# Optimization experiments

Hardware: AMD Instinct MI355X
Metric: run time of the kernel (lower is better)

## Reference

```python
import jax, jax.numpy as jnp
import numpy as np

WIDTH = 1024
NUM_BLOCKS = 16
BLOCK_W = WIDTH // NUM_BLOCKS
C_VALUE = 8.0
D_VALUE = 1.0
LN_EPS = 1e-6  # flax nn.LayerNorm default


def setup_inputs() -> dict:
    key = jax.random.key(0)
    kx, kw, ka = jax.random.split(key, 3)
    x = jax.random.normal(kx, (4, 8192, WIDTH), dtype=jnp.float32)
    # BlockDiagonalLinear params (variance_scaling fan_in normal ~ std=1/sqrt(block_w))
    w = jax.random.normal(kw, (NUM_BLOCKS, BLOCK_W, BLOCK_W), dtype=jnp.float32) / np.sqrt(BLOCK_W)
    b = jnp.zeros((NUM_BLOCKS, BLOCK_W), dtype=jnp.float32)
    # LayerNorm params
    ln_scale = jnp.ones((WIDTH,), dtype=jnp.float32)
    ln_bias = jnp.zeros((WIDTH,), dtype=jnp.float32)
    # a_param: rnn_param_init on ring [0.9, 0.999] with softplus transform
    unif = jax.random.uniform(ka, (WIDTH,))
    a_real = 0.5 * jnp.log(unif * (0.999 ** 2 - 0.9 ** 2) + 0.9 ** 2 + 1e-8)
    a_param = jnp.log(jnp.exp(-a_real) - 1.0).astype(jnp.float32)
    return {"x": x, "ln_scale": ln_scale, "ln_bias": ln_bias, "w": w, "b": b, "a_param": a_param}


def reference(x, ln_scale, ln_bias, w, b, a_param):
    # LayerNorm over last axis
    mean = jnp.mean(x, axis=-1, keepdims=True)
    var = jnp.mean(jnp.square(x - mean), axis=-1, keepdims=True)
    xn = (x - mean) * jax.lax.rsqrt(var + LN_EPS) * ln_scale + ln_bias
    # Block-diagonal linear: [..., (h i)] -> [..., h, i] @ [h, i, j] -> [..., (h j)]
    xb = xn.reshape(*xn.shape[:-1], NUM_BLOCKS, BLOCK_W)
    yb = jnp.einsum('bshi,hij->bshj', xb, w) + b
    gate_input = yb.reshape(*x.shape[:-1], WIDTH)
    # gate chain
    log_a = -C_VALUE * jax.nn.sigmoid(D_VALUE * gate_input) * jax.nn.softplus(a_param)
    alpha = jnp.exp(log_a)
    alpha = jnp.clip(alpha, 0.05, 0.95)  # gate_type == 'gru'
    beta = 1.0 - alpha
    return (alpha, beta)
```

## Files before the change

### kernel.cpp

```cpp
#include <hip/hip_runtime.h>

#define WIDTH 1024
#define BW 64
#define NB 16
#define ROWS 8
#define HPAD 68
#define ROWSTRIDE (NB * HPAD)

__global__ __launch_bounds__(512, 6)
void griffin_gate_kernel(const float* __restrict__ x,
                         const float* __restrict__ ln_scale,
                         const float* __restrict__ ln_bias,
                         const float* __restrict__ w,
                         const float* __restrict__ b,
                         const float* __restrict__ a_param,
                         float* __restrict__ alpha_out,
                         float* __restrict__ beta_out)
{
    __shared__ float xn_s[ROWS * ROWSTRIDE];

    const int t    = threadIdx.x;
    const int wave = t >> 6;
    const int lane = t & 63;
    const long long row_base = (long long)blockIdx.x * ROWS;

    const int h   = t >> 5;
    const int jl  = (t & 31) * 2;
    const int col = h * BW + jl;
    const float2 bias2 = *(const float2*)(b + col);
    const float2 ap    = *(const float2*)(a_param + col);
    float2 sp;
    sp.x = log1pf(__expf(ap.x));
    sp.y = log1pf(__expf(ap.y));

    {
        const float* xrow = x + (row_base + wave) * WIDTH;
        float4 v[4];
        float s = 0.f, s2 = 0.f;
#pragma unroll
        for (int k = 0; k < 4; ++k) {
            v[k] = *(const float4*)(xrow + 256 * k + 4 * lane);
            s += v[k].x + v[k].y + v[k].z + v[k].w;
            s2 = fmaf(v[k].x, v[k].x, s2);
            s2 = fmaf(v[k].y, v[k].y, s2);
            s2 = fmaf(v[k].z, v[k].z, s2);
            s2 = fmaf(v[k].w, v[k].w, s2);
        }
#pragma unroll
        for (int off = 32; off >= 1; off >>= 1) {
            s  += __shfl_xor(s,  off, 64);
            s2 += __shfl_xor(s2, off, 64);
        }
        const float mean = s * (1.0f / WIDTH);
        const float var  = fmaxf(s2 * (1.0f / WIDTH) - mean * mean, 0.0f);
        const float rstd = rsqrtf(var + 1e-6f);
#pragma unroll
        for (int k = 0; k < 4; ++k) {
            const float4 sc = *(const float4*)(ln_scale + 256 * k + 4 * lane);
            const float4 bi = *(const float4*)(ln_bias  + 256 * k + 4 * lane);
            float4 xn;
            xn.x = fmaf((v[k].x - mean) * rstd, sc.x, bi.x);
            xn.y = fmaf((v[k].y - mean) * rstd, sc.y, bi.y);
            xn.z = fmaf((v[k].z - mean) * rstd, sc.z, bi.z);
            xn.w = fmaf((v[k].w - mean) * rstd, sc.w, bi.w);
            const int hh    = 4 * k + (lane >> 4);
            const int inner = 4 * (lane & 15);
            *(float4*)(&xn_s[wave * ROWSTRIDE + hh * HPAD + inner]) = xn;
        }
    }
    __syncthreads();

    float2 acc[ROWS];
#pragma unroll
    for (int r = 0; r < ROWS; ++r) acc[r] = bias2;

    const float* wh = w + h * (BW * BW) + jl;
    const float* xs = xn_s + h * HPAD;
#pragma unroll 4
    for (int i4 = 0; i4 < 16; ++i4) {
        const float* wp = wh + i4 * 4 * BW;
        const float2 w0 = *(const float2*)(wp);
        const float2 w1 = *(const float2*)(wp + BW);
        const float2 w2 = *(const float2*)(wp + 2 * BW);
        const float2 w3 = *(const float2*)(wp + 3 * BW);
#pragma unroll
        for (int r = 0; r < ROWS; ++r) {
            const float4 xq = *(const float4*)(xs + r * ROWSTRIDE + i4 * 4);
            acc[r].x = fmaf(xq.x, w0.x, acc[r].x);
            acc[r].y = fmaf(xq.x, w0.y, acc[r].y);
            acc[r].x = fmaf(xq.y, w1.x, acc[r].x);
            acc[r].y = fmaf(xq.y, w1.y, acc[r].y);
            acc[r].x = fmaf(xq.z, w2.x, acc[r].x);
            acc[r].y = fmaf(xq.z, w2.y, acc[r].y);
            acc[r].x = fmaf(xq.w, w3.x, acc[r].x);
            acc[r].y = fmaf(xq.w, w3.y, acc[r].y);
        }
    }

    float* aout = alpha_out + row_base * WIDTH + col;
    float* bout = beta_out  + row_base * WIDTH + col;
#pragma unroll
    for (int r = 0; r < ROWS; ++r) {
        const float2 g = acc[r];
        float2 al;
        al.x = __expf(-8.0f * sp.x * __builtin_amdgcn_rcpf(1.0f + __expf(-g.x)));
        al.y = __expf(-8.0f * sp.y * __builtin_amdgcn_rcpf(1.0f + __expf(-g.y)));
        al.x = fminf(fmaxf(al.x, 0.05f), 0.95f);
        al.y = fminf(fmaxf(al.y, 0.05f), 0.95f);
        const float2 be = make_float2(1.0f - al.x, 1.0f - al.y);
        *(float2*)(aout + (long long)r * WIDTH) = al;
        *(float2*)(bout + (long long)r * WIDTH) = be;
    }
}

extern "C" void kernel_launch(void* const* d_in, const int* in_sizes, int n_in,
                              void* d_out, int out_size, void* d_ws, size_t ws_size,
                              hipStream_t stream)
{
    const float* x        = (const float*)d_in[0];
    const float* ln_scale = (const float*)d_in[1];
    const float* ln_bias  = (const float*)d_in[2];
    const float* w        = (const float*)d_in[3];
    const float* b        = (const float*)d_in[4];
    const float* a_param  = (const float*)d_in[5];

    const long long total = (long long)in_sizes[0];
    const long long rows  = total / WIDTH;
    float* alpha_out = (float*)d_out;
    float* beta_out  = alpha_out + total;

    const int grid = (int)(rows / ROWS);
    griffin_gate_kernel<<<grid, 512, 0, stream>>>(x, ln_scale, ln_bias, w, b, a_param,
                                                  alpha_out, beta_out);
}
```

Measured before the change: 432.9 us.

## Retile block-diagonal matmul to 4 rows x 4 columns per thread

Changes the per-thread work split in the block-diagonal GEMM from 8 rows x 2 columns to 4 rows x 4 columns, with two row groups of 256 threads. Each thread now does float4 weight loads and float4 output stores, and reads four LDS float4s per k-step instead of eight. The bias and softplus loads move after the loop, and launch bounds go from 6 to 8 blocks to push occupancy higher. The aim is to cut LDS read traffic per FMA and improve store width, at the cost of tighter register limits and reading each weight from global or L2 twice per block.

Result: no change. 428.1 us (-1.1%).

```diff
diff --git a/kernel.cpp b/kernel.cpp
--- a/kernel.cpp
+++ b/kernel.cpp
@@ -7,7 +7,7 @@
 #define HPAD 68
 #define ROWSTRIDE (NB * HPAD)
 
-__global__ __launch_bounds__(512, 6)
+__global__ __launch_bounds__(512, 8)
 void griffin_gate_kernel(const float* __restrict__ x,
                          const float* __restrict__ ln_scale,
                          const float* __restrict__ ln_bias,
@@ -23,15 +23,6 @@
     const int wave = t >> 6;
     const int lane = t & 63;
     const long long row_base = (long long)blockIdx.x * ROWS;
-
-    const int h   = t >> 5;
-    const int jl  = (t & 31) * 2;
-    const int col = h * BW + jl;
-    const float2 bias2 = *(const float2*)(b + col);
-    const float2 ap    = *(const float2*)(a_param + col);
-    float2 sp;
-    sp.x = log1pf(__expf(ap.x));
-    sp.y = log1pf(__expf(ap.y));
 
     {
         const float* xrow = x + (row_base + wave) * WIDTH;
@@ -70,46 +61,69 @@
     }
     __syncthreads();
 
-    float2 acc[ROWS];
+    const int rg  = t >> 8;
+    const int h   = (t & 255) >> 4;
+    const int jq  = t & 15;
+    const int col = h * BW + jq * 4;
+
+    float4 acc[4];
 #pragma unroll
-    for (int r = 0; r < ROWS; ++r) acc[r] = bias2;
+    for (int r = 0; r < 4; ++r) acc[r] = make_float4(0.f, 0.f, 0.f, 0.f);
 
-    const float* wh = w + h * (BW * BW) + jl;
-    const float* xs = xn_s + h * HPAD;
+    const float* wh = w + h * (BW * BW) + jq * 4;
+    const float* xs = xn_s + (rg * 4) * ROWSTRIDE + h * HPAD;
+
 #pragma unroll 4
     for (int i4 = 0; i4 < 16; ++i4) {
+        float4 xq0 = *(const float4*)(xs + 0 * ROWSTRIDE + i4 * 4);
+        float4 xq1 = *(const float4*)(xs + 1 * ROWSTRIDE + i4 * 4);
+        float4 xq2 = *(const float4*)(xs + 2 * ROWSTRIDE + i4 * 4);
+        float4 xq3 = *(const float4*)(xs + 3 * ROWSTRIDE + i4 * 4);
         const float* wp = wh + i4 * 4 * BW;
-        const float2 w0 = *(const float2*)(wp);
-        const float2 w1 = *(const float2*)(wp + BW);
-        const float2 w2 = *(const float2*)(wp + 2 * BW);
-        const float2 w3 = *(const float2*)(wp + 3 * BW);
 #pragma unroll
-        for (int r = 0; r < ROWS; ++r) {
-            const float4 xq = *(const float4*)(xs + r * ROWSTRIDE + i4 * 4);
-            acc[r].x = fmaf(xq.x, w0.x, acc[r].x);
-            acc[r].y = fmaf(xq.x, w0.y, acc[r].y);
-            acc[r].x = fmaf(xq.y, w1.x, acc[r].x);
-            acc[r].y = fmaf(xq.y, w1.y, acc[r].y);
-            acc[r].x = fmaf(xq.z, w2.x, acc[r].x);
-            acc[r].y = fmaf(xq.z, w2.y, acc[r].y);
-            acc[r].x = fmaf(xq.w, w3.x, acc[r].x);
-            acc[r].y = fmaf(xq.w, w3.y, acc[r].y);
+        for (int s = 0; s < 4; ++s) {
+            const float4 ws = *(const float4*)(wp + s * BW);
+            const float  x0 = (&xq0.x)[s], x1 = (&xq1.x)[s], x2 = (&xq2.x)[s], x3 = (&xq3.x)[s];
+            acc[0].x = fmaf(x0, ws.x, acc[0].x); acc[0].y = fmaf(x0, ws.y, acc[0].y);
+            acc[0].z = fmaf(x0, ws.z, acc[0].z); acc[0].w = fmaf(x0, ws.w, acc[0].w);
+            acc[1].x = fmaf(x1, ws.x, acc[1].x); acc[1].y = fmaf(x1, ws.y, acc[1].y);
+            acc[1].z = fmaf(x1, ws.z, acc[1].z); acc[1].w = fmaf(x1, ws.w, acc[1].w);
+            acc[2].x = fmaf(x2, ws.x, acc[2].x); acc[2].y = fmaf(x2, ws.y, acc[2].y);
+            acc[2].z = fmaf(x2, ws.z, acc[2].z); acc[2].w = fmaf(x2, ws.w, acc[2].w);
+            acc[3].x = fmaf(x3, ws.x, acc[3].x); acc[3].y = fmaf(x3, ws.y, acc[3].y);
+            acc[3].z = fmaf(x3, ws.z, acc[3].z); acc[3].w = fmaf(x3, ws.w, acc[3].w);
         }
     }
 
-    float* aout = alpha_out + row_base * WIDTH + col;
-    float* bout = beta_out  + row_base * WIDTH + col;
+    const float4 bias4 = *(const float4*)(b + col);
+    const float4 ap    = *(const float4*)(a_param + col);
+    float4 sp;
+    sp.x = log1pf(__expf(ap.x));
+    sp.y = log1pf(__expf(ap.y));
+    sp.z = log1pf(__expf(ap.z));
+    sp.w = log1pf(__expf(ap.w));
+
+    float* aout = alpha_out + (row_base + rg * 4) * WIDTH + col;
+    float* bout = beta_out  + (row_base + rg * 4) * WIDTH + col;
 #pragma unroll
-    for (int r = 0; r < ROWS; ++r) {
-        const float2 g = acc[r];
-        float2 al;
+    for (int r = 0; r < 4; ++r) {
+        float4 g;
+        g.x = acc[r].x + bias4.x;
+        g.y = acc[r].y + bias4.y;
+        g.z = acc[r].z + bias4.z;
+        g.w = acc[r].w + bias4.w;
+        float4 al;
         al.x = __expf(-8.0f * sp.x * __builtin_amdgcn_rcpf(1.0f + __expf(-g.x)));
         al.y = __expf(-8.0f * sp.y * __builtin_amdgcn_rcpf(1.0f + __expf(-g.y)));
+        al.z = __expf(-8.0f * sp.z * __builtin_amdgcn_rcpf(1.0f + __expf(-g.z)));
+        al.w = __expf(-8.0f * sp.w * __builtin_amdgcn_rcpf(1.0f + __expf(-g.w)));
         al.x = fminf(fmaxf(al.x, 0.05f), 0.95f);
         al.y = fminf(fmaxf(al.y, 0.05f), 0.95f);
-        const float2 be = make_float2(1.0f - al.x, 1.0f - al.y);
-        *(float2*)(aout + (long long)r * WIDTH) = al;
-        *(float2*)(bout + (long long)r * WIDTH) = be;
+        al.z = fminf(fmaxf(al.z, 0.05f), 0.95f);
+        al.w = fminf(fmaxf(al.w, 0.05f), 0.95f);
+        const float4 be = make_float4(1.0f - al.x, 1.0f - al.y, 1.0f - al.z, 1.0f - al.w);
+        *(float4*)(aout + (long long)r * WIDTH) = al;
+        *(float4*)(bout + (long long)r * WIDTH) = be;
     }
 }
 
```

## Compute block-diagonal matmul with bf16 MFMA and precompute weights in prep kernel

Applied to the files above, without the earlier changes.

Replaces the FP32 scalar FMA block-diagonal matmul with bf16 16x16x32 MFMA instructions. LayerNorm output is stored as bf16 in a swizzled shared-memory layout. A small prep kernel converts the weights into the MFMA operand layout and precomputes -8*softplus(a_param) into workspace. Each block now handles 16 rows. The aim is to remove the FP32 FMA and LDS bottleneck, at the cost of bf16 rounding of activations and weights and an extra kernel launch.

Result: faster. 415.1 us (-4.1%).

```diff
diff --git a/kernel.cpp b/kernel.cpp
--- a/kernel.cpp
+++ b/kernel.cpp
@@ -1,50 +1,68 @@
 #include <hip/hip_runtime.h>
+#include <hip/hip_bf16.h>
 
 #define WIDTH 1024
 #define BW 64
 #define NB 16
-#define ROWS 8
-#define HPAD 68
-#define ROWSTRIDE (NB * HPAD)
+#define ROWS 16
+
+typedef __attribute__((ext_vector_type(8))) __bf16 bf16x8;
+typedef __attribute__((ext_vector_type(4))) float f32x4;
+typedef __attribute__((ext_vector_type(4))) unsigned short u16x4;
+typedef __attribute__((ext_vector_type(8))) unsigned short u16x8;
+
+__device__ __forceinline__ unsigned short f2bf(float f) {
+    __hip_bfloat16 h = __float2bfloat16(f);
+    return __builtin_bit_cast(unsigned short, h);
+}
+
+__global__ void prep_kernel(const float* __restrict__ w, const float* __restrict__ a_param,
+                            unsigned short* __restrict__ wbf, float* __restrict__ msp) {
+    const int tid = blockIdx.x * 256 + threadIdx.x;
+    const int h = tid >> 9, m = (tid >> 7) & 3, s = (tid >> 6) & 1, l = tid & 63;
+    const int j  = m * 16 + (l & 15);
+    const int i0 = s * 32 + ((l >> 4) << 3);
+    const float* wp = w + h * (BW * BW) + i0 * BW + j;
+    u16x8 o;
+#pragma unroll
+    for (int e = 0; e < 8; ++e) o[e] = f2bf(wp[e * BW]);
+    *(u16x8*)(wbf + (long long)tid * 8) = o;
+    if (tid < WIDTH) {
+        msp[tid] = -8.0f * log1pf(__expf(a_param[tid]));
+    }
+}
 
 __global__ __launch_bounds__(512, 6)
 void griffin_gate_kernel(const float* __restrict__ x,
                          const float* __restrict__ ln_scale,
                          const float* __restrict__ ln_bias,
-                         const float* __restrict__ w,
                          const float* __restrict__ b,
-                         const float* __restrict__ a_param,
+                         const unsigned short* __restrict__ wbf,
+                         const float* __restrict__ msp,
                          float* __restrict__ alpha_out,
                          float* __restrict__ beta_out)
 {
-    __shared__ float xn_s[ROWS * ROWSTRIDE];
+    __shared__ unsigned short xn_s[ROWS * WIDTH];
 
-    const int t    = threadIdx.x;
-    const int wave = t >> 6;
-    const int lane = t & 63;
-    const long long row_base = (long long)blockIdx.x * ROWS;
+    const int t  = threadIdx.x;
+    const int wv = t >> 6;
+    const int l  = t & 63;
+    const long long base = (long long)blockIdx.x * ROWS;
 
-    const int h   = t >> 5;
-    const int jl  = (t & 31) * 2;
-    const int col = h * BW + jl;
-    const float2 bias2 = *(const float2*)(b + col);
-    const float2 ap    = *(const float2*)(a_param + col);
-    float2 sp;
-    sp.x = log1pf(__expf(ap.x));
-    sp.y = log1pf(__expf(ap.y));
-
-    {
-        const float* xrow = x + (row_base + wave) * WIDTH;
+#pragma unroll
+    for (int rr = 0; rr < 2; ++rr) {
+        const int tok = wv * 2 + rr;
+        const float* xrow = x + (base + tok) * WIDTH;
         float4 v[4];
         float s = 0.f, s2 = 0.f;
 #pragma unroll
-        for (int k = 0; k < 4; ++k) {
-            v[k] = *(const float4*)(xrow + 256 * k + 4 * lane);
-            s += v[k].x + v[k].y + v[k].z + v[k].w;
-            s2 = fmaf(v[k].x, v[k].x, s2);
-            s2 = fmaf(v[k].y, v[k].y, s2);
-            s2 = fmaf(v[k].z, v[k].z, s2);
-            s2 = fmaf(v[k].w, v[k].w, s2);
+        for (int c = 0; c < 4; ++c) {
+            v[c] = *(const float4*)(xrow + 256 * c + 4 * l);
+            s += v[c].x + v[c].y + v[c].z + v[c].w;
+            s2 = fmaf(v[c].x, v[c].x, s2);
+            s2 = fmaf(v[c].y, v[c].y, s2);
+            s2 = fmaf(v[c].z, v[c].z, s2);
+            s2 = fmaf(v[c].w, v[c].w, s2);
         }
 #pragma unroll
         for (int off = 32; off >= 1; off >>= 1) {
@@ -54,62 +72,60 @@
         const float mean = s * (1.0f / WIDTH);
         const float var  = fmaxf(s2 * (1.0f / WIDTH) - mean * mean, 0.0f);
         const float rstd = rsqrtf(var + 1e-6f);
+        char* rowp = (char*)(xn_s + tok * WIDTH);
+        const int swz = (tok & 7) << 4;
 #pragma unroll
-        for (int k = 0; k < 4; ++k) {
-            const float4 sc = *(const float4*)(ln_scale + 256 * k + 4 * lane);
-            const float4 bi = *(const float4*)(ln_bias  + 256 * k + 4 * lane);
-            float4 xn;
-            xn.x = fmaf((v[k].x - mean) * rstd, sc.x, bi.x);
-            xn.y = fmaf((v[k].y - mean) * rstd, sc.y, bi.y);
-            xn.z = fmaf((v[k].z - mean) * rstd, sc.z, bi.z);
-            xn.w = fmaf((v[k].w - mean) * rstd, sc.w, bi.w);
-            const int hh    = 4 * k + (lane >> 4);
-            const int inner = 4 * (lane & 15);
-            *(float4*)(&xn_s[wave * ROWSTRIDE + hh * HPAD + inner]) = xn;
+        for (int c = 0; c < 4; ++c) {
+            const float4 sc = *(const float4*)(ln_scale + 256 * c + 4 * l);
+            const float4 bi = *(const float4*)(ln_bias  + 256 * c + 4 * l);
+            u16x4 p;
+            p[0] = f2bf(fmaf((v[c].x - mean) * rstd, sc.x, bi.x));
+            p[1] = f2bf(fmaf((v[c].y - mean) * rstd, sc.y, bi.y));
+            p[2] = f2bf(fmaf((v[c].z - mean) * rstd, sc.z, bi.z));
+            p[3] = f2bf(fmaf((v[c].w - mean) * rstd, sc.w, bi.w));
+            *(u16x4*)(rowp + ((512 * c + 8 * l) ^ swz)) = p;
         }
     }
     __syncthreads();
 
-    float2 acc[ROWS];
+    const int tokc = l & 15;
+    const int g    = l >> 4;
+    const char* xb   = (const char*)(xn_s + tokc * WIDTH);
+    const int   swzr = (tokc & 7) << 4;
+    float* aout = alpha_out + (base + tokc) * WIDTH;
+    float* bout = beta_out  + (base + tokc) * WIDTH;
+
 #pragma unroll
-    for (int r = 0; r < ROWS; ++r) acc[r] = bias2;
+    for (int hh = 0; hh < 2; ++hh) {
+        const int h = wv * 2 + hh;
+        const bf16x8 b0 = *(const bf16x8*)(xb + ((h * 128 +  0 + g * 16) ^ swzr));
+        const bf16x8 b1 = *(const bf16x8*)(xb + ((h * 128 + 64 + g * 16) ^ swzr));
+        const u16x8* wb = (const u16x8*)wbf + h * 512 + l;
 
-    const float* wh = w + h * (BW * BW) + jl;
-    const float* xs = xn_s + h * HPAD;
-#pragma unroll 4
-    for (int i4 = 0; i4 < 16; ++i4) {
-        const float* wp = wh + i4 * 4 * BW;
-        const float2 w0 = *(const float2*)(wp);
-        const float2 w1 = *(const float2*)(wp + BW);
-        const float2 w2 = *(const float2*)(wp + 2 * BW);
-        const float2 w3 = *(const float2*)(wp + 3 * BW);
 #pragma unroll
-        for (int r = 0; r < ROWS; ++r) {
-            const float4 xq = *(const float4*)(xs + r * ROWSTRIDE + i4 * 4);
-            acc[r].x = fmaf(xq.x, w0.x, acc[r].x);
-            acc[r].y = fmaf(xq.x, w0.y, acc[r].y);
-            acc[r].x = fmaf(xq.y, w1.x, acc[r].x);
-            acc[r].y = fmaf(xq.y, w1.y, acc[r].y);
-            acc[r].x = fmaf(xq.z, w2.x, acc[r].x);
-            acc[r].y = fmaf(xq.z, w2.y, acc[r].y);
-            acc[r].x = fmaf(xq.w, w3.x, acc[r].x);
-            acc[r].y = fmaf(xq.w, w3.y, acc[r].y);
+        for (int m = 0; m < 4; ++m) {
+            f32x4 acc = {0.f, 0.f, 0.f, 0.f};
+            acc = __builtin_amdgcn_mfma_f32_16x16x32_bf16(
+                      __builtin_bit_cast(bf16x8, wb[(m * 2 + 0) * 64]), b0, acc, 0, 0, 0);
+            acc = __builtin_amdgcn_mfma_f32_16x16x32_bf16(
+                      __builtin_bit_cast(bf16x8, wb[(m * 2 + 1) * 64]), b1, acc, 0, 0, 0);
+
+            const int jbase = h * 64 + m * 16 + g * 4;
+            const float4 bias4 = *(const float4*)(b   + jbase);
+            const float4 ms4   = *(const float4*)(msp + jbase);
+            float4 al, be;
+#pragma unroll
+            for (int e = 0; e < 4; ++e) {
+                const float gt  = acc[e] + (&bias4.x)[e];
+                const float sig = __builtin_amdgcn_rcpf(1.0f + __expf(-gt));
+                float a = __expf((&ms4.x)[e] * sig);
+                a = fminf(fmaxf(a, 0.05f), 0.95f);
+                (&al.x)[e] = a;
+                (&be.x)[e] = 1.0f - a;
+            }
+            *(float4*)(aout + jbase) = al;
+            *(float4*)(bout + jbase) = be;
         }
-    }
-
-    float* aout = alpha_out + row_base * WIDTH + col;
-    float* bout = beta_out  + row_base * WIDTH + col;
-#pragma unroll
-    for (int r = 0; r < ROWS; ++r) {
-        const float2 g = acc[r];
-        float2 al;
-        al.x = __expf(-8.0f * sp.x * __builtin_amdgcn_rcpf(1.0f + __expf(-g.x)));
-        al.y = __expf(-8.0f * sp.y * __builtin_amdgcn_rcpf(1.0f + __expf(-g.y)));
-        al.x = fminf(fmaxf(al.x, 0.05f), 0.95f);
-        al.y = fminf(fmaxf(al.y, 0.05f), 0.95f);
-        const float2 be = make_float2(1.0f - al.x, 1.0f - al.y);
-        *(float2*)(aout + (long long)r * WIDTH) = al;
-        *(float2*)(bout + (long long)r * WIDTH) = be;
     }
 }
 
@@ -129,7 +145,11 @@
     float* alpha_out = (float*)d_out;
     float* beta_out  = alpha_out + total;
 
+    unsigned short* wbf = (unsigned short*)d_ws;
+    float*          msp = (float*)((char*)d_ws + NB * BW * BW * 2);
+
+    prep_kernel<<<32, 256, 0, stream>>>(w, a_param, wbf, msp);
     const int grid = (int)(rows / ROWS);
-    griffin_gate_kernel<<<grid, 512, 0, stream>>>(x, ln_scale, ln_bias, w, b, a_param,
+    griffin_gate_kernel<<<grid, 512, 0, stream>>>(x, ln_scale, ln_bias, b, wbf, msp,
                                                   alpha_out, beta_out);
 }
```
